# Performance work log

Hardware: AMD Instinct MI355X
Metric: run time of the kernel (lower is better)

The kernel has to match this reference:

```python
import jax, jax.numpy as jnp
import numpy as np

BB, F, K, D, H, HFF, L, M_PREV = 128, 8, 256, 256, 256, 512, 2, 2


def setup_inputs() -> dict:
    key = jax.random.key(0)
    ks = jax.random.split(key, 16)
    f32 = jnp.float32

    def lin(k, fan_in, shape):
        return (jax.random.normal(k, shape, dtype=f32) / np.sqrt(fan_in)).astype(f32)

    inp = {
        "x_BD": jax.random.normal(ks[0], (BB, D), dtype=f32),
        "xhat_BFD": jax.random.normal(ks[1], (BB, F, D), dtype=f32),
        "codes_MBF": jax.random.randint(ks[2], (M_PREV, BB, 1), 0, F * K, dtype=jnp.int64),
        "codebook": jax.random.normal(ks[3], (K, D), dtype=f32) / np.sqrt(D),
        "W_in": lin(ks[4], D, (D, H)),
        "b_in": jnp.zeros((H,), f32),
        # concat projection over cat([h, xhat], -1): (H + D) -> H
        "W_cat": lin(ks[5], H + D, (H + D, H)),
        "b_cat": jnp.zeros((H,), f32),
        "W1": lin(ks[6], H, (L, H, HFF)),
        "b1": jnp.zeros((L, HFF), f32),
        "W2": lin(ks[7], HFF, (L, HFF, H)),
        "b2": jnp.zeros((L, H), f32),
        "W_out": lin(ks[8], H, (H, D)),
        "b_out": jnp.zeros((D,), f32),
    }
    return inp


def reference(x_BD, xhat_BFD, codes_MBF, codebook, W_in, b_in, W_cat, b_cat,
              W1, b1, W2, b2, W_out, b_out):
    Bb, Fb, Dd = xhat_BFD.shape
    Kk = codebook.shape[0]

    # in_proj applied to the (shared) codebook once: [K, H]
    h0 = codebook @ W_in + b_in

    # concat(h, xhat) as a linear over the concatenation, split to avoid
    # materializing a [Bb,F,K,H+D] tensor.
    Wc, Wx = W_cat[:H], W_cat[H:]
    h = (h0 @ Wc)[None, None] + (xhat_BFD @ Wx)[:, :, None] + b_cat  # [Bb,F,K,H]

    # residual MLP blocks: h <- h + W2 relu(W1 h)
    for l in range(L):
        h = h + jax.nn.relu(h @ W1[l] + b1[l]) @ W2[l] + b2[l]

    # out_proj + residual codeword (res_codeword_coeff = 1.0) + xhat offset
    cw = h @ W_out + b_out + codebook[None, None]        # [Bb,F,K,D]
    cw = cw + xhat_BFD[:, :, None]                        # reconstructed candidates

    cflat = cw.reshape(Bb, Fb * Kk, Dd)                   # [Bb, F*K, D]

    dists = (jnp.sum(x_BD * x_BD, -1, keepdims=True)
             - 2.0 * jnp.einsum('bd,bkd->bk', x_BD, cflat)
             + jnp.sum(cflat * cflat, -1))                # [Bb, F*K]

    idx = jnp.argmin(dists, axis=-1)                      # [Bb]
    xhat_next_BFD = jnp.take_along_axis(cflat, idx[:, None, None], axis=1)  # [Bb,1,D]

    codes_new = jnp.concatenate(
        [codes_MBF, idx[None, :, None].astype(codes_MBF.dtype)], axis=0)
    return xhat_next_BFD, codes_new
```

## Files before the change

kernel.cpp:

```cpp
#include <hip/hip_runtime.h>
#include <hip/hip_bf16.h>

#define B_   128
#define F_   8
#define K_   256
#define D_   256
#define H_   256
#define HFF_ 512
#define RT   64

typedef _Float16 half8  __attribute__((ext_vector_type(8)));
typedef _Float16 half4v __attribute__((ext_vector_type(4)));
typedef float floatx4   __attribute__((ext_vector_type(4)));

#define MFMAH(a,b,c) __builtin_amdgcn_mfma_f32_16x16x32_f16(a,b,c,0,0,0)

#define HA_S  260
#define HMA_S 132

__global__ void k_prep(const float* __restrict__ cb, const float* __restrict__ Win,
                       const float* __restrict__ bin, const float* __restrict__ Wcat,
                       const float* __restrict__ bcat, const float* __restrict__ xhat,
                       const float* __restrict__ W1, const float* __restrict__ W2,
                       const float* __restrict__ Wout,
                       float* __restrict__ u, float* __restrict__ v,
                       _Float16* __restrict__ w1f, _Float16* __restrict__ w2f,
                       _Float16* __restrict__ wof) {
  const int blk = blockIdx.x, t = threadIdx.x;
  if (blk < K_) {
    __shared__ float row[D_];
    __shared__ float h0row[H_];
    row[t] = cb[blk * D_ + t];
    __syncthreads();
    float acc = bin[t];
    #pragma unroll 4
    for (int i = 0; i < D_; ++i) acc = fmaf(row[i], Win[i * H_ + t], acc);
    h0row[t] = acc;
    __syncthreads();
    float acc2 = 0.f;
    #pragma unroll 4
    for (int i = 0; i < H_; ++i) acc2 = fmaf(h0row[i], Wcat[i * H_ + t], acc2);
    u[blk * H_ + t] = acc2;
  } else if (blk < K_ + B_ * F_) {
    __shared__ float row2[D_];
    const int bf = blk - K_;
    row2[t] = xhat[bf * D_ + t];
    __syncthreads();
    float acc = bcat[t];
    #pragma unroll 4
    for (int i = 0; i < D_; ++i) acc = fmaf(row2[i], Wcat[(H_ + i) * H_ + t], acc);
    v[bf * H_ + t] = acc;
  } else {
    const int e = (blk - (K_ + B_ * F_)) * 256 + t;
    const float* src; _Float16* dst; int N, NT, le;
    if (e < 262144) {
      const int layer = e >> 17; le = e & 131071;
      src = W1 + layer * (H_ * HFF_); dst = w1f + layer * (H_ * HFF_);
      N = HFF_; NT = 32;
    } else if (e < 524288) {
      const int e2 = e - 262144;
      const int layer = e2 >> 17; le = e2 & 131071;
      src = W2 + layer * (HFF_ * H_); dst = w2f + layer * (HFF_ * H_);
      N = H_; NT = 16;
    } else {
      le = e - 524288; src = Wout; dst = wof; N = D_; NT = 16;
    }
    const int jj = le & 7, lane = (le >> 3) & 63, r = le >> 9;
    const int ntile = r % NT, kstep = r / NT;
    const int row = kstep * 32 + (lane >> 4) * 8 + jj;
    const int colc = ntile * 16 + (lane & 15);
    dst[le] = (_Float16)src[row * N + colc];
  }
}

__global__ __launch_bounds__(256, 3) void k_main(
    const float* __restrict__ u, const float* __restrict__ v,
    const _Float16* __restrict__ w1f, const float* __restrict__ b1,
    const _Float16* __restrict__ w2f, const float* __restrict__ b2,
    const _Float16* __restrict__ woutf, const float* __restrict__ bout,
    const float* __restrict__ cb, const float* __restrict__ xhat,
    const float* __restrict__ x, float* __restrict__ dists) {
  __shared__ _Float16 hA[64][HA_S];
  __shared__ _Float16 hmA[64][HMA_S];
  __shared__ float x_s[D_], xh_s[D_];
  __shared__ float dist_s[4][64];

  const int t = threadIdx.x;
  const int blk = blockIdx.x;
  const int bf = blk >> 2, k0 = (blk & 3) << 6;
  const int b = bf >> 3, f = bf & 7;
  const int wave = t >> 6, lane = t & 63;
  const int col = lane & 15, quad = lane >> 4;
  const int lane8 = lane * 8;

  x_s[t]  = x[b * D_ + t];
  xh_s[t] = xhat[bf * D_ + t];

  {
    const int r = t >> 2, c0 = (t & 3) * 64;
    const float* up = u + (k0 + r) * H_ + c0;
    const float* vp = v + bf * H_ + c0;
    #pragma unroll
    for (int j = 0; j < 64; j += 8) {
      float4 uA = *(const float4*)(up + j);
      float4 vA = *(const float4*)(vp + j);
      float4 uB = *(const float4*)(up + j + 4);
      float4 vB = *(const float4*)(vp + j + 4);
      half8 hv8;
      hv8[0] = (_Float16)(uA.x + vA.x); hv8[1] = (_Float16)(uA.y + vA.y);
      hv8[2] = (_Float16)(uA.z + vA.z); hv8[3] = (_Float16)(uA.w + vA.w);
      hv8[4] = (_Float16)(uB.x + vB.x); hv8[5] = (_Float16)(uB.y + vB.y);
      hv8[6] = (_Float16)(uB.z + vB.z); hv8[7] = (_Float16)(uB.w + vB.w);
      *(half8*)&hA[r][c0 + j] = hv8;
    }
  }
  __syncthreads();

  const floatx4 zero4 = {0.f, 0.f, 0.f, 0.f};

  #pragma unroll 1
  for (int l = 0; l < 2; ++l) {
    const _Float16* w1_l = w1f + l * (H_ * HFF_);
    const _Float16* w2_l = w2f + l * (HFF_ * H_);
    const float* b1l = b1 + l * HFF_;
    const float* b2l = b2 + l * H_;

    floatx4 acc2[4][4];
    #pragma unroll
    for (int mt = 0; mt < 4; ++mt)
      #pragma unroll
      for (int nt = 0; nt < 4; ++nt) acc2[mt][nt] = zero4;

    #pragma unroll 1
    for (int ch = 0; ch < 4; ++ch) {
      floatx4 acc1[2][4];
      #pragma unroll
      for (int mt = 0; mt < 2; ++mt)
        #pragma unroll
        for (int nt = 0; nt < 4; ++nt) acc1[mt][nt] = zero4;

      const _Float16* w1_b = w1_l + (ch * 8 + wave * 2) * 512 + lane8;

      #pragma unroll 4
      for (int ks = 0; ks < 8; ++ks) {
        half8 b0 = *(const half8*)&hA[col][ks * 32 + quad * 8];
        half8 b1v = *(const half8*)&hA[16 + col][ks * 32 + quad * 8];
        half8 b2v = *(const half8*)&hA[32 + col][ks * 32 + quad * 8];
        half8 b3v = *(const half8*)&hA[48 + col][ks * 32 + quad * 8];
        const int ko = ks * 32 * 512;
        #pragma unroll
        for (int mt = 0; mt < 2; ++mt) {
          half8 aw = *(const half8*)(w1_b + ko + mt * 512);
          acc1[mt][0] = MFMAH(aw, b0, acc1[mt][0]);
          acc1[mt][1] = MFMAH(aw, b1v, acc1[mt][1]);
          acc1[mt][2] = MFMAH(aw, b2v, acc1[mt][2]);
          acc1[mt][3] = MFMAH(aw, b3v, acc1[mt][3]);
        }
      }
      #pragma unroll
      for (int mt = 0; mt < 2; ++mt) {
        const int floc = (wave * 2 + mt) * 16 + quad * 4;
        float4 bb = *(const float4*)&b1l[ch * 128 + floc];
        #pragma unroll
        for (int nt = 0; nt < 4; ++nt) {
          const int row = nt * 16 + col;
          half4v nh;
          #pragma unroll
          for (int p = 0; p < 4; ++p)
            nh[p] = (_Float16)fmaxf(acc1[mt][nt][p] + ((const float*)&bb)[p], 0.f);
          *(half4v*)&hmA[row][floc] = nh;
        }
      }
      __syncthreads();

      const _Float16* w2_b = w2_l + (ch * 64 + wave * 4) * 512 + lane8;
      #pragma unroll 2
      for (int ks = 0; ks < 4; ++ks) {
        half8 b0 = *(const half8*)&hmA[col][ks * 32 + quad * 8];
        half8 b1v = *(const half8*)&hmA[16 + col][ks * 32 + quad * 8];
        half8 b2v = *(const half8*)&hmA[32 + col][ks * 32 + quad * 8];
        half8 b3v = *(const half8*)&hmA[48 + col][ks * 32 + quad * 8];
        const int ko = ks * 16 * 512;
        #pragma unroll
        for (int mt = 0; mt < 4; ++mt) {
          half8 aw = *(const half8*)(w2_b + ko + mt * 512);
          acc2[mt][0] = MFMAH(aw, b0, acc2[mt][0]);
          acc2[mt][1] = MFMAH(aw, b1v, acc2[mt][1]);
          acc2[mt][2] = MFMAH(aw, b2v, acc2[mt][2]);
          acc2[mt][3] = MFMAH(aw, b3v, acc2[mt][3]);
        }
      }
      __syncthreads();
    }

    #pragma unroll
    for (int mt = 0; mt < 4; ++mt) {
      const int feat0 = (wave * 4 + mt) * 16 + quad * 4;
      float4 bb = *(const float4*)&b2l[feat0];
      #pragma unroll
      for (int nt = 0; nt < 4; ++nt) {
        const int row = nt * 16 + col;
        half4v oh = *(half4v*)&hA[row][feat0];
        half4v nh;
        #pragma unroll
        for (int p = 0; p < 4; ++p)
          nh[p] = (_Float16)((float)oh[p] + acc2[mt][nt][p] + ((const float*)&bb)[p]);
        *(half4v*)&hA[row][feat0] = nh;
      }
    }
    __syncthreads();
  }

  floatx4 acc3[4][4];
  #pragma unroll
  for (int mt = 0; mt < 4; ++mt)
    #pragma unroll
    for (int nt = 0; nt < 4; ++nt) acc3[mt][nt] = zero4;

  const _Float16* wo_b = woutf + (wave * 4) * 512 + lane8;
  #pragma unroll 2
  for (int ks = 0; ks < 8; ++ks) {
    half8 b0 = *(const half8*)&hA[col][ks * 32 + quad * 8];
    half8 b1v = *(const half8*)&hA[16 + col][ks * 32 + quad * 8];
    half8 b2v = *(const half8*)&hA[32 + col][ks * 32 + quad * 8];
    half8 b3v = *(const half8*)&hA[48 + col][ks * 32 + quad * 8];
    const int ko = ks * 16 * 512;
    #pragma unroll
    for (int mt = 0; mt < 4; ++mt) {
      half8 aw = *(const half8*)(wo_b + ko + mt * 512);
      acc3[mt][0] = MFMAH(aw, b0, acc3[mt][0]);
      acc3[mt][1] = MFMAH(aw, b1v, acc3[mt][1]);
      acc3[mt][2] = MFMAH(aw, b2v, acc3[mt][2]);
      acc3[mt][3] = MFMAH(aw, b3v, acc3[mt][3]);
    }
  }

  float s[4] = {0.f, 0.f, 0.f, 0.f};
  #pragma unroll
  for (int mt = 0; mt < 4; ++mt) {
    const int d0 = (wave * 4 + mt) * 16 + quad * 4;
    float4 bo = *(const float4*)&bout[d0];
    float4 xv = *(const float4*)&x_s[d0];
    float4 xh4 = *(const float4*)&xh_s[d0];
    #pragma unroll
    for (int nt = 0; nt < 4; ++nt) {
      float4 cbv = *(const float4*)&cb[(k0 + nt * 16 + col) * D_ + d0];
      #pragma unroll
      for (int p = 0; p < 4; ++p) {
        float base = ((const float*)&bo)[p] + ((const float*)&xh4)[p];
        float xx = ((const float*)&xv)[p];
        float cw = acc3[mt][nt][p] + base + ((const float*)&cbv)[p];
        s[nt] += cw * (cw - 2.f * xx);
      }
    }
  }
  #pragma unroll
  for (int nt = 0; nt < 4; ++nt) {
    s[nt] += __shfl_xor(s[nt], 16, 64);
    s[nt] += __shfl_xor(s[nt], 32, 64);
  }
  if (quad == 0) {
    #pragma unroll
    for (int nt = 0; nt < 4; ++nt)
      dist_s[wave][nt * 16 + col] = s[nt];
  }
  __syncthreads();
  if (t < 64) {
    float d = dist_s[0][t] + dist_s[1][t] + dist_s[2][t] + dist_s[3][t];
    dists[b * (F_ * K_) + f * K_ + k0 + t] = d;
  }
}

__global__ void k_top8(const float* __restrict__ dists, int* __restrict__ topi) {
  __shared__ float ds[F_ * K_];
  __shared__ float bv[256];
  __shared__ int bi_s[256];
  const int b = blockIdx.x, t = threadIdx.x;
  for (int j = t; j < F_ * K_; j += 256) ds[j] = dists[b * (F_ * K_) + j];
  __syncthreads();
  for (int pass = 0; pass < 8; ++pass) {
    float best = 3.4e38f; int bi = 0;
    for (int j = t; j < F_ * K_; j += 256) {
      const float dv = ds[j];
      if (dv < best) { best = dv; bi = j; }
    }
    bv[t] = best; bi_s[t] = bi;
    __syncthreads();
    for (int s = 128; s > 0; s >>= 1) {
      if (t < s) {
        const float ov = bv[t + s]; const int oi = bi_s[t + s];
        if (ov < bv[t] || (ov == bv[t] && oi < bi_s[t])) { bv[t] = ov; bi_s[t] = oi; }
      }
      __syncthreads();
    }
    if (t == 0) { topi[b * 8 + pass] = bi_s[0]; ds[bi_s[0]] = 3.4e38f; }
    __syncthreads();
  }
}

#define NCL 2
__global__ __launch_bounds__(512) void k_resfin(
    const float* __restrict__ u, const float* __restrict__ v,
    const float* __restrict__ W1, const float* __restrict__ b1,
    const float* __restrict__ W2, const float* __restrict__ b2,
    const float* __restrict__ Wout, const float* __restrict__ bout,
    const float* __restrict__ cb, const float* __restrict__ xhat,
    const float* __restrict__ x, const int* __restrict__ topi,
    float* __restrict__ resc2, int* __restrict__ iwin2,
    float* __restrict__ cwhalf) {
  __shared__ float hs4[4][H_ + 4];
  __shared__ float hms4[4][HFF_ + 4];
  __shared__ float cw4[4][H_ + 4];
  __shared__ float redw[8][NCL];
  __shared__ int   sel_sh;

  const int blk = blockIdx.x;
  const int b = blk >> 1, half = blk & 1;
  const int t = threadIdx.x;
  const int g = t >> 8, tloc = t & 255;
  const int wave = t >> 6, lane = t & 63;
  const int cbase = half * 4;

  int kc[NCL], bfc[NCL];
  #pragma unroll
  for (int cl = 0; cl < NCL; ++cl) {
    const int ix = topi[b * 8 + cbase + g * 2 + cl];
    kc[cl] = ix & 255;
    bfc[cl] = b * F_ + (ix >> 8);
  }

  #pragma unroll
  for (int cl = 0; cl < NCL; ++cl)
    hs4[g * 2 + cl][tloc] = u[kc[cl] * H_ + tloc] + v[bfc[cl] * H_ + tloc];
  __syncthreads();

  #pragma unroll 1
  for (int l = 0; l < 2; ++l) {
    const float* W1l = W1 + l * (H_ * HFF_);
    const float* W2l = W2 + l * (HFF_ * H_);

    float a0[NCL], a1[NCL];
    {
      const float bb0 = b1[l * HFF_ + tloc], bb1 = b1[l * HFF_ + 256 + tloc];
      #pragma unroll
      for (int cl = 0; cl < NCL; ++cl) { a0[cl] = bb0; a1[cl] = bb1; }
    }
    #pragma unroll 2
    for (int i = 0; i < H_; i += 4) {
      float4 hv[NCL];
      #pragma unroll
      for (int cl = 0; cl < NCL; ++cl) hv[cl] = *(const float4*)&hs4[g * 2 + cl][i];
      #pragma unroll
      for (int q = 0; q < 4; ++q) {
        const float w0 = W1l[(i + q) * HFF_ + tloc];
        const float w1 = W1l[(i + q) * HFF_ + 256 + tloc];
        #pragma unroll
        for (int cl = 0; cl < NCL; ++cl) {
          const float h = ((const float*)&hv[cl])[q];
          a0[cl] = fmaf(h, w0, a0[cl]);
          a1[cl] = fmaf(h, w1, a1[cl]);
        }
      }
    }
    #pragma unroll
    for (int cl = 0; cl < NCL; ++cl) {
      hms4[g * 2 + cl][tloc] = fmaxf(a0[cl], 0.f);
      hms4[g * 2 + cl][tloc + 256] = fmaxf(a1[cl], 0.f);
    }
    __syncthreads();

    float hn[NCL];
    {
      const float bb2 = b2[l * H_ + tloc];
      #pragma unroll
      for (int cl = 0; cl < NCL; ++cl) hn[cl] = hs4[g * 2 + cl][tloc] + bb2;
    }
    #pragma unroll 2
    for (int jj = 0; jj < HFF_; jj += 4) {
      float4 hv[NCL];
      #pragma unroll
      for (int cl = 0; cl < NCL; ++cl) hv[cl] = *(const float4*)&hms4[g * 2 + cl][jj];
      #pragma unroll
      for (int q = 0; q < 4; ++q) {
        const float w = W2l[(jj + q) * H_ + tloc];
        #pragma unroll
        for (int cl = 0; cl < NCL; ++cl)
          hn[cl] = fmaf(((const float*)&hv[cl])[q], w, hn[cl]);
      }
    }
    __syncthreads();
    #pragma unroll
    for (int cl = 0; cl < NCL; ++cl) hs4[g * 2 + cl][tloc] = hn[cl];
    __syncthreads();
  }

  float cw[NCL];
  {
    const float bo = bout[tloc];
    #pragma unroll
    for (int cl = 0; cl < NCL; ++cl)
      cw[cl] = bo + cb[kc[cl] * D_ + tloc] + xhat[bfc[cl] * D_ + tloc];
  }
  #pragma unroll 2
  for (int i = 0; i < H_; i += 4) {
    float4 hv[NCL];
    #pragma unroll
    for (int cl = 0; cl < NCL; ++cl) hv[cl] = *(const float4*)&hs4[g * 2 + cl][i];
    #pragma unroll
    for (int q = 0; q < 4; ++q) {
      const float w = Wout[(i + q) * D_ + tloc];
      #pragma unroll
      for (int cl = 0; cl < NCL; ++cl)
        cw[cl] = fmaf(((const float*)&hv[cl])[q], w, cw[cl]);
    }
  }

  const float xx = x[b * D_ + tloc];
  #pragma unroll
  for (int cl = 0; cl < NCL; ++cl) {
    cw4[g * 2 + cl][tloc] = cw[cl];
    float vsum = cw[cl] * (cw[cl] - 2.f * xx);
    vsum += __shfl_xor(vsum, 1, 64);
    vsum += __shfl_xor(vsum, 2, 64);
    vsum += __shfl_xor(vsum, 4, 64);
    vsum += __shfl_xor(vsum, 8, 64);
    vsum += __shfl_xor(vsum, 16, 64);
    vsum += __shfl_xor(vsum, 32, 64);
    if (lane == 0) redw[wave][cl] = vsum;
  }
  __syncthreads();
  if (t == 0) {
    float bd = 3.4e38f; int bidx = 1 << 30; int bc = 0;
    #pragma unroll
    for (int c = 0; c < 4; ++c) {
      const int gg = c >> 1, cl = c & 1;
      const float d = redw[gg * 4 + 0][cl] + redw[gg * 4 + 1][cl] +
                      redw[gg * 4 + 2][cl] + redw[gg * 4 + 3][cl];
      const int ix = topi[b * 8 + cbase + c];
      if (d < bd || (d == bd && ix < bidx)) { bd = d; bidx = ix; bc = c; }
    }
    resc2[blk] = bd;
    iwin2[blk] = bidx;
    sel_sh = bc;
  }
  __syncthreads();
  if (t < 256) cwhalf[blk * 256 + t] = cw4[sel_sh][t];
}

__global__ void k_finw(const float* __restrict__ resc2, const int* __restrict__ iwin2,
                       const float* __restrict__ cwhalf, const int* __restrict__ codes,
                       float* __restrict__ out) {
  const int b = blockIdx.x, t = threadIdx.x;
  const float d0 = resc2[b * 2], d1 = resc2[b * 2 + 1];
  const int i0 = iwin2[b * 2], i1 = iwin2[b * 2 + 1];
  const int sel = (d1 < d0 || (d1 == d0 && i1 < i0)) ? 1 : 0;
  out[b * D_ + t] = cwhalf[(b * 2 + sel) * 256 + t];
  if (t < 2)
    out[B_ * D_ + t * B_ + b] = (float)codes[t * B_ + b];
  else if (t == 2)
    out[B_ * D_ + 2 * B_ + b] = (float)(sel ? i1 : i0);
}

extern "C" void kernel_launch(void* const* d_in, const int* in_sizes, int n_in,
                              void* d_out, int out_size, void* d_ws, size_t ws_size,
                              hipStream_t stream) {
  const float* x    = (const float*)d_in[0];
  const float* xhat = (const float*)d_in[1];
  const int*   codes= (const int*)d_in[2];
  const float* cb   = (const float*)d_in[3];
  const float* Win  = (const float*)d_in[4];
  const float* bin  = (const float*)d_in[5];
  const float* Wcat = (const float*)d_in[6];
  const float* bcat = (const float*)d_in[7];
  const float* W1   = (const float*)d_in[8];
  const float* b1   = (const float*)d_in[9];
  const float* W2   = (const float*)d_in[10];
  const float* b2   = (const float*)d_in[11];
  const float* Wout = (const float*)d_in[12];
  const float* bout = (const float*)d_in[13];
  float* out = (float*)d_out;

  float* u     = (float*)d_ws;
  float* v     = u + K_ * H_;
  float* dists = v + B_ * F_ * H_;
  float* resc  = dists + B_ * F_ * K_;
  int*   topi  = (int*)(resc + 1024);
  int*   pad   = topi + 1024;
  _Float16* w1f  = (_Float16*)(pad + 128);
  _Float16* w2f  = w1f + 2 * H_ * HFF_;
  _Float16* wof  = w2f + 2 * HFF_ * H_;

  float* resc2  = resc;
  int*   iwin2  = (int*)(resc + 256);
  float* cwhalf = dists;

  k_prep<<<K_ + B_ * F_ + 2304, 256, 0, stream>>>(cb, Win, bin, Wcat, bcat, xhat,
                                                  W1, W2, Wout, u, v, w1f, w2f, wof);

  k_main<<<B_ * F_ * (K_ / RT), 256, 0, stream>>>(u, v, w1f, b1, w2f, b2,
                                                  wof, bout, cb, xhat, x, dists);
  k_top8<<<B_, 256, 0, stream>>>(dists, topi);
  k_resfin<<<2 * B_, 512, 0, stream>>>(u, v, W1, b1, W2, b2, Wout, bout, cb, xhat,
                                       x, topi, resc2, iwin2, cwhalf);
  k_finw<<<B_, 256, 0, stream>>>(resc2, iwin2, cwhalf, codes, out);
}
```

Measured before the change: 541.1 us.

## Split prep dot products into four accumulators, raise MFMA wave priority, widen top8 block

The prep kernel's serial FMA chains are split into four independent accumulators so more loads and FMAs can be in flight at once. s_setprio is raised around the MFMA loops in the main kernel to favour waves issuing matrix instructions. The top-8 selection kernel now runs with 512 threads, which halves each thread's scan length but adds one more reduction step. The accumulator split also changes the floating-point summation order slightly.

```diff
diff --git a/kernel.cpp b/kernel.cpp
--- a/kernel.cpp
+++ b/kernel.cpp
@@ -32,24 +32,39 @@
     __shared__ float h0row[H_];
     row[t] = cb[blk * D_ + t];
     __syncthreads();
-    float acc = bin[t];
+    float a0 = 0.f, a1 = 0.f, a2 = 0.f, a3 = 0.f;
     #pragma unroll 4
-    for (int i = 0; i < D_; ++i) acc = fmaf(row[i], Win[i * H_ + t], acc);
-    h0row[t] = acc;
-    __syncthreads();
-    float acc2 = 0.f;
+    for (int i = 0; i < 64; ++i) {
+      a0 = fmaf(row[i      ], Win[(i      ) * H_ + t], a0);
+      a1 = fmaf(row[i +  64], Win[(i +  64) * H_ + t], a1);
+      a2 = fmaf(row[i + 128], Win[(i + 128) * H_ + t], a2);
+      a3 = fmaf(row[i + 192], Win[(i + 192) * H_ + t], a3);
+    }
+    h0row[t] = bin[t] + ((a0 + a1) + (a2 + a3));
+    __syncthreads();
+    float c0 = 0.f, c1 = 0.f, c2 = 0.f, c3 = 0.f;
     #pragma unroll 4
-    for (int i = 0; i < H_; ++i) acc2 = fmaf(h0row[i], Wcat[i * H_ + t], acc2);
-    u[blk * H_ + t] = acc2;
+    for (int i = 0; i < 64; ++i) {
+      c0 = fmaf(h0row[i      ], Wcat[(i      ) * H_ + t], c0);
+      c1 = fmaf(h0row[i +  64], Wcat[(i +  64) * H_ + t], c1);
+      c2 = fmaf(h0row[i + 128], Wcat[(i + 128) * H_ + t], c2);
+      c3 = fmaf(h0row[i + 192], Wcat[(i + 192) * H_ + t], c3);
+    }
+    u[blk * H_ + t] = (c0 + c1) + (c2 + c3);
   } else if (blk < K_ + B_ * F_) {
     __shared__ float row2[D_];
     const int bf = blk - K_;
     row2[t] = xhat[bf * D_ + t];
     __syncthreads();
-    float acc = bcat[t];
+    float a0 = 0.f, a1 = 0.f, a2 = 0.f, a3 = 0.f;
     #pragma unroll 4
-    for (int i = 0; i < D_; ++i) acc = fmaf(row2[i], Wcat[(H_ + i) * H_ + t], acc);
-    v[bf * H_ + t] = acc;
+    for (int i = 0; i < 64; ++i) {
+      a0 = fmaf(row2[i      ], Wcat[(H_ + i      ) * H_ + t], a0);
+      a1 = fmaf(row2[i +  64], Wcat[(H_ + i +  64) * H_ + t], a1);
+      a2 = fmaf(row2[i + 128], Wcat[(H_ + i + 128) * H_ + t], a2);
+      a3 = fmaf(row2[i + 192], Wcat[(H_ + i + 192) * H_ + t], a3);
+    }
+    v[bf * H_ + t] = bcat[t] + ((a0 + a1) + (a2 + a3));
   } else {
     const int e = (blk - (K_ + B_ * F_)) * 256 + t;
     const float* src; _Float16* dst; int N, NT, le;
@@ -141,6 +156,7 @@
 
       const _Float16* w1_b = w1_l + (ch * 8 + wave * 2) * 512 + lane8;
 
+      __builtin_amdgcn_s_setprio(1);
       #pragma unroll 4
       for (int ks = 0; ks < 8; ++ks) {
         half8 b0 = *(const half8*)&hA[col][ks * 32 + quad * 8];
@@ -157,6 +173,7 @@
           acc1[mt][3] = MFMAH(aw, b3v, acc1[mt][3]);
         }
       }
+      __builtin_amdgcn_s_setprio(0);
       #pragma unroll
       for (int mt = 0; mt < 2; ++mt) {
         const int floc = (wave * 2 + mt) * 16 + quad * 4;
@@ -174,6 +191,7 @@
       __syncthreads();
 
       const _Float16* w2_b = w2_l + (ch * 64 + wave * 4) * 512 + lane8;
+      __builtin_amdgcn_s_setprio(1);
       #pragma unroll 2
       for (int ks = 0; ks < 4; ++ks) {
         half8 b0 = *(const half8*)&hmA[col][ks * 32 + quad * 8];
@@ -190,6 +208,7 @@
           acc2[mt][3] = MFMAH(aw, b3v, acc2[mt][3]);
         }
       }
+      __builtin_amdgcn_s_setprio(0);
       __syncthreads();
     }
 
@@ -218,6 +237,7 @@
     for (int nt = 0; nt < 4; ++nt) acc3[mt][nt] = zero4;
 
   const _Float16* wo_b = woutf + (wave * 4) * 512 + lane8;
+  __builtin_amdgcn_s_setprio(1);
   #pragma unroll 2
   for (int ks = 0; ks < 8; ++ks) {
     half8 b0 = *(const half8*)&hA[col][ks * 32 + quad * 8];
@@ -234,6 +254,7 @@
       acc3[mt][3] = MFMAH(aw, b3v, acc3[mt][3]);
     }
   }
+  __builtin_amdgcn_s_setprio(0);
 
   float s[4] = {0.f, 0.f, 0.f, 0.f};
   #pragma unroll
@@ -273,20 +294,20 @@
 
 __global__ void k_top8(const float* __restrict__ dists, int* __restrict__ topi) {
   __shared__ float ds[F_ * K_];
-  __shared__ float bv[256];
-  __shared__ int bi_s[256];
+  __shared__ float bv[512];
+  __shared__ int bi_s[512];
   const int b = blockIdx.x, t = threadIdx.x;
-  for (int j = t; j < F_ * K_; j += 256) ds[j] = dists[b * (F_ * K_) + j];
+  for (int j = t; j < F_ * K_; j += 512) ds[j] = dists[b * (F_ * K_) + j];
   __syncthreads();
   for (int pass = 0; pass < 8; ++pass) {
     float best = 3.4e38f; int bi = 0;
-    for (int j = t; j < F_ * K_; j += 256) {
+    for (int j = t; j < F_ * K_; j += 512) {
       const float dv = ds[j];
       if (dv < best) { best = dv; bi = j; }
     }
     bv[t] = best; bi_s[t] = bi;
     __syncthreads();
-    for (int s = 128; s > 0; s >>= 1) {
+    for (int s = 256; s > 0; s >>= 1) {
       if (t < s) {
         const float ov = bv[t + s]; const int oi = bi_s[t + s];
         if (ov < bv[t] || (ov == bv[t] && oi < bi_s[t])) { bv[t] = ov; bi_s[t] = oi; }
@@ -499,7 +520,7 @@
 
   k_main<<<B_ * F_ * (K_ / RT), 256, 0, stream>>>(u, v, w1f, b1, w2f, b2,
                                                   wof, bout, cb, xhat, x, dists);
-  k_top8<<<B_, 256, 0, stream>>>(dists, topi);
+  k_top8<<<B_, 512, 0, stream>>>(dists, topi);
   k_resfin<<<2 * B_, 512, 0, stream>>>(u, v, W1, b1, W2, b2, Wout, bout, cb, xhat,
                                        x, topi, resc2, iwin2, cwhalf);
   k_finw<<<B_, 256, 0, stream>>>(resc2, iwin2, cwhalf, codes, out);
```

Measured after the change: 521.9 us. 1.04x faster.
